# Kernel tuning notes

Hardware: AMD Instinct MI355X
Metric: run time of the kernel (lower is better)

## Reference

```python
import jax, jax.numpy as jnp
import numpy as np
import math

B, N = 1, 512
C_S, C_Z, C_H, H = 384, 128, 16, 12
P_Q, P_V, NBINS = 4, 8, 64
OUT_DIM = H * (C_H + P_V * 4 + C_Z)


def setup_inputs() -> dict:
    key = jax.random.key(0)
    ks = jax.random.split(key, 16)
    def rn(k, shape, scale=1.0):
        return jax.random.normal(k, shape, dtype=jnp.float32) * scale
    rotations, _ = jnp.linalg.qr(rn(ks[3], (B, N, 3, 3)))  # orthogonal frames
    w = 0.02
    return {
        "s": rn(ks[0], (B, N, C_S)),
        "z": rn(ks[1], (B, N, N, C_Z)),
        "translations": rn(ks[2], (B, N, 3), 10.0),  # spread over ~0-32 A bins
        "rotations": rotations,
        "Wq": rn(ks[4], (C_S, H * C_H), w), "bq": jnp.zeros((H * C_H,), jnp.float32),
        "Wk": rn(ks[5], (C_S, H * C_H), w), "bk": jnp.zeros((H * C_H,), jnp.float32),
        "Wv": rn(ks[6], (C_S, H * C_H), w), "bv": jnp.zeros((H * C_H,), jnp.float32),
        "Wqp": rn(ks[7], (C_S, H * P_Q * 3), w), "bqp": jnp.zeros((H * P_Q * 3,), jnp.float32),
        "Wkp": rn(ks[8], (C_S, H * P_Q * 3), w), "bkp": jnp.zeros((H * P_Q * 3,), jnp.float32),
        "Wvp": rn(ks[9], (C_S, H * P_V * 3), w), "bvp": jnp.zeros((H * P_V * 3,), jnp.float32),
        "Wb": rn(ks[10], (C_Z, H), w), "bb": jnp.zeros((H,), jnp.float32),
        "emb": rn(ks[11], (NBINS, H), w),
        "scale_logits": jnp.zeros((3, H), jnp.float32),
        "head_weights": jnp.ones((H,), jnp.float32),
        "Wout": rn(ks[12], (OUT_DIM, C_S), w), "bout": jnp.zeros((C_S,), jnp.float32),
    }


def reference(s, z, translations, rotations, Wq, bq, Wk, bk, Wv, bv, Wqp, bqp, Wkp, bkp, Wvp, bvp, Wb, bb, emb, scale_logits, head_weights, Wout, bout):
    b, n, _ = s.shape
    t = translations
    q = (s @ Wq + bq).reshape(b, n, H, C_H)
    k = (s @ Wk + bk).reshape(b, n, H, C_H)
    v = (s @ Wv + bv).reshape(b, n, H, C_H)
    q_pts = (s @ Wqp + bqp).reshape(b, n, H, P_Q, 3)
    k_pts = (s @ Wkp + bkp).reshape(b, n, H, P_Q, 3)
    v_pts = (s @ Wvp + bvp).reshape(b, n, H, P_V, 3)
    # local -> global frame
    q_g = jnp.einsum('bnij,bnhpj->bnhpi', rotations, q_pts) + t[:, :, None, None, :]
    k_g = jnp.einsum('bnij,bnhpj->bnhpi', rotations, k_pts) + t[:, :, None, None, :]
    v_g = jnp.einsum('bnij,bnhpj->bnhpi', rotations, v_pts) + t[:, :, None, None, :]
    scalar_logits = jnp.einsum('bnhc,bmhc->bnmh', q, k) / math.sqrt(C_H)  # [b,n,m,h]
    point_dist = jnp.sum((q_g[:, :, None] - k_g[:, None]) ** 2, axis=-1)  # [b,n,m,h,p]
    point_logits = -0.5 * jnp.sum(point_dist, axis=-1) * head_weights[None, None, None, :]
    pair_bias = z @ Wb + bb  # [b,n,m,h]
    pair_dist = jnp.linalg.norm(t[:, :, None, :] - t[:, None, :, :], axis=-1)  # [b,n,m]
    edges = jnp.linspace(0.0, 32.0, NBINS + 1)
    bins = jnp.clip(jnp.searchsorted(edges, pair_dist, side='left') - 1, 0, NBINS - 1)
    dist_bias = emb[bins]  # [b,n,m,h]
    scales = jnp.stack([
        (pair_dist <= 5.0).astype(s.dtype),
        ((pair_dist > 5.0) & (pair_dist <= 15.0)).astype(s.dtype),
        jnp.ones_like(pair_dist),
    ], axis=-1)  # [b,n,m,3]
    per_head = jax.nn.softmax(scale_logits, axis=0)  # [3,h]
    multiscale = jnp.einsum('bnms,sh->bnmh', scales, per_head)
    logits = scalar_logits + point_logits + pair_bias + dist_bias + multiscale
    attn = jax.nn.softmax(logits.astype(jnp.float32), axis=2).astype(s.dtype)  # over m
    out_scalar = jnp.einsum('bnmh,bmhc->bnhc', attn, v)
    out_pts_g = jnp.einsum('bnmh,bmhpi->bnhpi', attn, v_g)
    # global -> local frame (R^T applied)
    out_pts_l = jnp.einsum('bnji,bnhpj->bnhpi', rotations, out_pts_g - t[:, :, None, None, :])
    out_norms = jnp.linalg.norm(out_pts_l, axis=-1)  # [b,n,h,p]
    pair_feat = jnp.einsum('bnmh,bnmc->bnhc', attn, z)
    feats = jnp.concatenate([
        out_scalar,
        out_pts_l.reshape(b, n, H, P_V * 3),
        out_norms,
        pair_feat,
    ], axis=-1).reshape(b, n, -1)  # [b,n,OUT_DIM]
    return feats @ Wout + bout
```

## Files before the change

### kernel.cpp

```cpp
#include <hip/hip_runtime.h>

#define NTOK 512
#define CS 384
#define CZ 128
#define CH 16
#define HN 12
#define PQ 4
#define PV 8
#define FEAT_DIM 2112
#define HSEG 176

__global__ __launch_bounds__(256) void k_proj(
    const float* __restrict__ s,
    const float* __restrict__ Wq,  const float* __restrict__ bq,
    const float* __restrict__ Wk,  const float* __restrict__ bk,
    const float* __restrict__ Wv,  const float* __restrict__ bv,
    const float* __restrict__ Wqp, const float* __restrict__ bqp,
    const float* __restrict__ Wkp, const float* __restrict__ bkp,
    const float* __restrict__ Wvp, const float* __restrict__ bvp,
    float* __restrict__ qs, float* __restrict__ ks, float* __restrict__ vs,
    float* __restrict__ raw_g)
{
    __shared__ float s_l[16 * CS];
    const int t  = threadIdx.x;
    const int n0 = blockIdx.x * 16;

    const float4* sg  = (const float4*)(s + (size_t)n0 * CS);
    float4*       sl4 = (float4*)s_l;
#pragma unroll
    for (int j = 0; j < 6; ++j) sl4[j * 256 + t] = sg[j * 256 + t];
    __syncthreads();

    const int col = blockIdx.y * 64 + (t & 63);
    const int tq  = t >> 6;

    const float *W, *bv_;
    int lc, nc;
    if (col < 192)      { W = Wq;  bv_ = bq;  lc = col;       nc = 192; }
    else if (col < 384) { W = Wk;  bv_ = bk;  lc = col - 192; nc = 192; }
    else if (col < 576) { W = Wv;  bv_ = bv;  lc = col - 384; nc = 192; }
    else if (col < 720) { W = Wqp; bv_ = bqp; lc = col - 576; nc = 144; }
    else if (col < 864) { W = Wkp; bv_ = bkp; lc = col - 720; nc = 144; }
    else                { W = Wvp; bv_ = bvp; lc = col - 864; nc = 288; }

    const float* Wp   = W + lc;
    const float* srow = s_l + tq * 4 * CS;
    float a0, a1, a2, a3;
    a0 = a1 = a2 = a3 = bv_[lc];
#pragma unroll 8
    for (int k = 0; k < CS; ++k) {
        float w = Wp[(size_t)k * nc];
        a0 += srow[k] * w;
        a1 += srow[CS + k] * w;
        a2 += srow[2 * CS + k] * w;
        a3 += srow[3 * CS + k] * w;
    }

    const int n = n0 + tq * 4;
    if (col < 576) {
        float* dst = (col < 192 ? qs : col < 384 ? ks : vs);
        dst[(size_t)(n + 0) * 192 + lc] = a0;
        dst[(size_t)(n + 1) * 192 + lc] = a1;
        dst[(size_t)(n + 2) * 192 + lc] = a2;
        dst[(size_t)(n + 3) * 192 + lc] = a3;
    } else {
        const int pc = col - 576;
        raw_g[(size_t)(n + 0) * 576 + pc] = a0;
        raw_g[(size_t)(n + 1) * 576 + pc] = a1;
        raw_g[(size_t)(n + 2) * 576 + pc] = a2;
        raw_g[(size_t)(n + 3) * 576 + pc] = a3;
    }
}

__global__ __launch_bounds__(256) void k_frame(
    const float* __restrict__ raw_g,
    const float* __restrict__ trans,
    const float* __restrict__ rot,
    float* __restrict__ qg, float* __restrict__ kg, float* __restrict__ vg)
{
    const int e = blockIdx.x * 256 + threadIdx.x;
    const int n = e / 576, loc = e % 576;
    const int i = loc % 3, base = loc - i;
    const float* rp = raw_g + (size_t)n * 576 + base;
    float x0 = rp[0], x1 = rp[1], x2 = rp[2];
    const float* R = rot + (size_t)n * 9 + i * 3;
    float v = trans[(size_t)n * 3 + i] + R[0] * x0 + R[1] * x1 + R[2] * x2;
    if (loc < 144)      qg[(size_t)n * 144 + loc] = v;
    else if (loc < 288) kg[(size_t)n * 144 + loc - 144] = v;
    else                vg[(size_t)n * 288 + loc - 288] = v;
}

__global__ __launch_bounds__(256) void k_bias(
    const float* __restrict__ z,
    const float* __restrict__ Wb,
    const float* __restrict__ bbv,
    float* __restrict__ bias)
{
    __shared__ float a_l[64 * 132];
    __shared__ float wb_l[CZ * HN];
    __shared__ float bb_l[HN];
    const int t = threadIdx.x;
    for (int i = t; i < CZ * HN; i += 256) wb_l[i] = Wb[i];
    if (t < HN) bb_l[t] = bbv[t];

    const float4* zg = (const float4*)(z + (size_t)blockIdx.x * 64 * CZ);
#pragma unroll
    for (int j = 0; j < 8; ++j) {
        const int f4i = j * 256 + t;
        const int row = f4i >> 5, c4 = f4i & 31;
        *(float4*)&a_l[row * 132 + c4 * 4] = zg[f4i];
    }
    __syncthreads();

    const int row = t & 63;
    const int hg  = t >> 6;
    float acc0 = 0.f, acc1 = 0.f, acc2 = 0.f;
    const float4* ar = (const float4*)&a_l[row * 132];
    const float*  wr = wb_l + hg * 3;
#pragma unroll 8
    for (int k4 = 0; k4 < 32; ++k4) {
        float4 zv = ar[k4];
        float zs[4] = {zv.x, zv.y, zv.z, zv.w};
#pragma unroll
        for (int e = 0; e < 4; ++e) {
            const float* w = wr + (k4 * 4 + e) * HN;
            acc0 += zs[e] * w[0];
            acc1 += zs[e] * w[1];
            acc2 += zs[e] * w[2];
        }
    }
    const int grow = blockIdx.x * 64 + row;
    const int n = grow >> 9, m = grow & 511;
    const int h = hg * 3;
    bias[((size_t)n * HN + h + 0) * NTOK + m] = acc0 + bb_l[h + 0];
    bias[((size_t)n * HN + h + 1) * NTOK + m] = acc1 + bb_l[h + 1];
    bias[((size_t)n * HN + h + 2) * NTOK + m] = acc2 + bb_l[h + 2];
}

__global__ __launch_bounds__(256) void k_attn(
    const float* __restrict__ qs, const float* __restrict__ ks,
    const float* __restrict__ qg, const float* __restrict__ kg,
    const float* __restrict__ trans,
    const float* __restrict__ emb,
    const float* __restrict__ slog,
    const float* __restrict__ hw,
    float* __restrict__ attn)
{
    const int n = blockIdx.x, h = blockIdx.y, t = threadIdx.x;
    __shared__ float ql[CH];
    __shared__ float qgl[12];
    __shared__ float tl[3];
    __shared__ float ph[3];
    __shared__ float red[8];
    if (t < CH)       ql[t] = qs[(size_t)n * 192 + h * CH + t];
    else if (t < 28)  qgl[t - 16] = qg[(size_t)n * 144 + h * 12 + (t - 16)];
    else if (t < 31)  tl[t - 28] = trans[(size_t)n * 3 + (t - 28)];
    else if (t == 31) {
        float s0 = slog[0 * HN + h], s1 = slog[1 * HN + h], s2 = slog[2 * HN + h];
        float mx = fmaxf(s0, fmaxf(s1, s2));
        float e0 = expf(s0 - mx), e1 = expf(s1 - mx), e2 = expf(s2 - mx);
        float inv = 1.f / (e0 + e1 + e2);
        ph[0] = e0 * inv; ph[1] = e1 * inv; ph[2] = e2 * inv;
    }
    __syncthreads();

    const float hwv = hw[h];
    float* arow = attn + ((size_t)n * HN + h) * NTOK;
    float lg[2];
#pragma unroll
    for (int r = 0; r < 2; ++r) {
        const int m = t + r * 256;
        const float4* kp4 = (const float4*)(ks + (size_t)m * 192 + h * CH);
        const float4* ql4 = (const float4*)ql;
        float sc = 0.f;
#pragma unroll
        for (int c = 0; c < 4; ++c) {
            float4 kv = kp4[c], qv = ql4[c];
            sc += qv.x * kv.x + qv.y * kv.y + qv.z * kv.z + qv.w * kv.w;
        }
        sc *= 0.25f;
        const float4* kg4 = (const float4*)(kg + (size_t)m * 144 + h * 12);
        const float4* qg4 = (const float4*)qgl;
        float sd = 0.f;
#pragma unroll
        for (int u = 0; u < 3; ++u) {
            float4 kv = kg4[u], qv = qg4[u];
            float d0 = qv.x - kv.x, d1 = qv.y - kv.y, d2 = qv.z - kv.z, d3 = qv.w - kv.w;
            sd += d0 * d0 + d1 * d1 + d2 * d2 + d3 * d3;
        }
        float pl = -0.5f * sd * hwv;
        float dx = tl[0] - trans[(size_t)m * 3 + 0];
        float dy = tl[1] - trans[(size_t)m * 3 + 1];
        float dz = tl[2] - trans[(size_t)m * 3 + 2];
        float dist = sqrtf(dx * dx + dy * dy + dz * dz);
        int bin = (int)ceilf(dist * 2.f) - 1;
        bin = min(63, max(0, bin));
        float db = emb[bin * HN + h];
        float ms = ph[2] + (dist <= 5.f ? ph[0] : 0.f) + ((dist > 5.f && dist <= 15.f) ? ph[1] : 0.f);
        lg[r] = sc + pl + arow[m] + db + ms;
    }

    float mx = fmaxf(lg[0], lg[1]);
    for (int off = 32; off; off >>= 1) mx = fmaxf(mx, __shfl_down(mx, off));
    if ((t & 63) == 0) red[t >> 6] = mx;
    __syncthreads();
    if (t == 0) red[4] = fmaxf(fmaxf(red[0], red[1]), fmaxf(red[2], red[3]));
    __syncthreads();
    mx = red[4];
    float e0 = expf(lg[0] - mx), e1 = expf(lg[1] - mx);
    float sm = e0 + e1;
    for (int off = 32; off; off >>= 1) sm += __shfl_down(sm, off);
    if ((t & 63) == 0) red[t >> 6] = sm;
    __syncthreads();
    if (t == 0) red[5] = red[0] + red[1] + red[2] + red[3];
    __syncthreads();
    const float inv = 1.f / red[5];
    arow[t] = e0 * inv;
    arow[t + 256] = e1 * inv;
}

__global__ __launch_bounds__(256) void k_out_partial(
    const float* __restrict__ attn,
    const float* __restrict__ vs, const float* __restrict__ vg,
    float* __restrict__ sums_g)
{
    __shared__ float a_l[HN * 128];
    const int n = blockIdx.x, mc = blockIdx.y, t = threadIdx.x;
    for (int i = t; i < HN * 128; i += 256) {
        const int h = i >> 7, mm = i & 127;
        a_l[i] = attn[((size_t)n * HN + h) * NTOK + mc * 128 + mm];
    }
    __syncthreads();

    const int mbase = mc * 128;
    const int o0 = t;
    const int o1raw = t + 256;
    const bool act1 = o1raw < 480;
    const int o1 = act1 ? o1raw : 0;
    const int h0 = o0 / 40, j0 = o0 % 40;
    const int h1 = o1 / 40, j1 = o1 % 40;
    const float* b0; int st0;
    if (j0 < 16) { b0 = vs + h0 * 16 + j0;        st0 = 192; }
    else         { b0 = vg + h0 * 24 + (j0 - 16); st0 = 288; }
    const float* b1; int st1;
    if (j1 < 16) { b1 = vs + h1 * 16 + j1;        st1 = 192; }
    else         { b1 = vg + h1 * 24 + (j1 - 16); st1 = 288; }
    b0 += (size_t)mbase * st0;
    b1 += (size_t)mbase * st1;
    const float* a0 = a_l + h0 * 128;
    const float* a1 = a_l + h1 * 128;
    float acc0 = 0.f, acc1 = 0.f;
#pragma unroll 8
    for (int m = 0; m < 128; ++m) {
        acc0 += a0[m] * b0[(size_t)m * st0];
        acc1 += a1[m] * b1[(size_t)m * st1];
    }
    atomicAdd(&sums_g[(size_t)n * 480 + o0], acc0);
    if (act1) atomicAdd(&sums_g[(size_t)n * 480 + o1raw], acc1);
}

__global__ __launch_bounds__(256) void k_out_epi(
    const float* __restrict__ sums_g,
    const float* __restrict__ trans,
    const float* __restrict__ rot,
    float* __restrict__ feats)
{
    __shared__ float sums[480];
    __shared__ float Rl[9];
    __shared__ float tl[3];
    const int n = blockIdx.x, t = threadIdx.x;
    for (int i = t; i < 480; i += 256) sums[i] = sums_g[(size_t)n * 480 + i];
    if (t < 9)       Rl[t] = rot[(size_t)n * 9 + t];
    else if (t < 12) tl[t - 9] = trans[(size_t)n * 3 + (t - 9)];
    __syncthreads();

    for (int f = t; f < 576; f += 256) {
        const int h = f / 48, j = f % 48;
        float* fp = feats + (size_t)n * FEAT_DIM + h * HSEG;
        const float* sh = sums + h * 40;
        if (j < 16) {
            fp[j] = sh[j];
        } else if (j < 40) {
            int jj = j - 16, p = jj / 3, i = jj % 3;
            float val = 0.f;
#pragma unroll
            for (int q = 0; q < 3; ++q) val += Rl[q * 3 + i] * (sh[16 + p * 3 + q] - tl[q]);
            fp[16 + jj] = val;
        } else {
            int p = j - 40;
            float s2 = 0.f;
#pragma unroll
            for (int i = 0; i < 3; ++i) {
                float val = 0.f;
#pragma unroll
                for (int q = 0; q < 3; ++q) val += Rl[q * 3 + i] * (sh[16 + p * 3 + q] - tl[q]);
                s2 += val * val;
            }
            fp[40 + p] = sqrtf(s2);
        }
    }
}

__global__ __launch_bounds__(256) void k_pairfeat(
    const float* __restrict__ attn,
    const float* __restrict__ z,
    float* __restrict__ feats)
{
    __shared__ float a_l[HN * NTOK];
    const int n = blockIdx.x, t = threadIdx.x;
    for (int i = t; i < HN * NTOK; i += 256) a_l[i] = attn[(size_t)n * HN * NTOK + i];
    __syncthreads();

    const int c2 = (t & 63) * 2;
    const int hb = (t >> 6) * 3;
    float acc[3][2] = {{0.f, 0.f}, {0.f, 0.f}, {0.f, 0.f}};
    const float* zp = z + (size_t)n * NTOK * CZ + c2;
    const float* ap = a_l + hb * NTOK;
#pragma unroll 4
    for (int m = 0; m < NTOK; ++m) {
        float2 zv = *(const float2*)(zp + (size_t)m * CZ);
#pragma unroll
        for (int u = 0; u < 3; ++u) {
            float a = ap[u * NTOK + m];
            acc[u][0] += a * zv.x;
            acc[u][1] += a * zv.y;
        }
    }
#pragma unroll
    for (int u = 0; u < 3; ++u) {
        float2 r = make_float2(acc[u][0], acc[u][1]);
        *(float2*)&feats[(size_t)n * FEAT_DIM + (hb + u) * HSEG + 48 + c2] = r;
    }
}

#define KT 16
__global__ __launch_bounds__(256) void k_outproj(
    const float* __restrict__ feats,
    const float* __restrict__ Wout,
    const float* __restrict__ bout,
    float* __restrict__ out)
{
    __shared__ float As[KT][64];
    __shared__ float Bs[KT][64];
    const int t  = threadIdx.x;
    const int n0 = blockIdx.x * 64;
    const int j0 = blockIdx.y * 64;
    const int k0 = blockIdx.z * HSEG;

    const int arow = t >> 2, akq = (t & 3) * 4;
    const int bkk  = t >> 4, bjq = (t & 15) * 4;
    const int tr   = t >> 4, tc  = t & 15;

    float acc[4][4] = {{0.f}};
    for (int s = 0; s < 11; ++s) {
        const int ks = k0 + s * KT;
        float4 a4 = *(const float4*)&feats[(size_t)(n0 + arow) * FEAT_DIM + ks + akq];
        float4 b4 = *(const float4*)&Wout[(size_t)(ks + bkk) * 384 + j0 + bjq];
        __syncthreads();
        As[akq + 0][arow] = a4.x;
        As[akq + 1][arow] = a4.y;
        As[akq + 2][arow] = a4.z;
        As[akq + 3][arow] = a4.w;
        *(float4*)&Bs[bkk][bjq] = b4;
        __syncthreads();
// ... 24 lines not shown
            atomicAdd(&out[(size_t)row * 384 + col], v);
        }
    }
}

extern "C" void kernel_launch(void* const* d_in, const int* in_sizes, int n_in,
                              void* d_out, int out_size, void* d_ws, size_t ws_size,
                              hipStream_t stream) {
    const float* s     = (const float*)d_in[0];
    const float* z     = (const float*)d_in[1];
    const float* trans = (const float*)d_in[2];
    const float* rot   = (const float*)d_in[3];
    const float* Wq    = (const float*)d_in[4];
    const float* bq    = (const float*)d_in[5];
    const float* Wk    = (const float*)d_in[6];
    const float* bk    = (const float*)d_in[7];
    const float* Wv    = (const float*)d_in[8];
    const float* bv    = (const float*)d_in[9];
    const float* Wqp   = (const float*)d_in[10];
    const float* bqp   = (const float*)d_in[11];
    const float* Wkp   = (const float*)d_in[12];
    const float* bkp   = (const float*)d_in[13];
    const float* Wvp   = (const float*)d_in[14];
    const float* bvp   = (const float*)d_in[15];
    const float* Wb    = (const float*)d_in[16];
    const float* bb    = (const float*)d_in[17];
    const float* emb   = (const float*)d_in[18];
    const float* slog  = (const float*)d_in[19];
    const float* hw    = (const float*)d_in[20];
    const float* Wout  = (const float*)d_in[21];
    const float* bout  = (const float*)d_in[22];

    float* W = (float*)d_ws;
    float* qs    = W;
    float* ks    = qs + 98304;
    float* vs    = ks + 98304;
    float* qg    = vs + 98304;
    float* kg    = qg + 73728;
    float* vg    = kg + 73728;
    float* bias  = vg + 147456;
    float* feats = bias + 3145728;
    float* raw_g = feats + 1081344;
    float* sums_g = raw_g;

    k_proj<<<dim3(32, 18), 256, 0, stream>>>(s, Wq, bq, Wk, bk, Wv, bv,
                                             Wqp, bqp, Wkp, bkp, Wvp, bvp,
                                             qs, ks, vs, raw_g);
    k_frame<<<1152, 256, 0, stream>>>(raw_g, trans, rot, qg, kg, vg);
    hipMemsetAsync(sums_g, 0, (size_t)NTOK * 480 * sizeof(float), stream);
    k_bias<<<4096, 256, 0, stream>>>(z, Wb, bb, bias);
    k_attn<<<dim3(512, 12), 256, 0, stream>>>(qs, ks, qg, kg, trans, emb, slog, hw, bias);
    k_out_partial<<<dim3(512, 4), 256, 0, stream>>>(bias, vs, vg, sums_g);
    k_out_epi<<<512, 256, 0, stream>>>(sums_g, trans, rot, feats);
    k_pairfeat<<<512, 256, 0, stream>>>(bias, z, feats);
    hipMemsetAsync(d_out, 0, (size_t)NTOK * 384 * sizeof(float), stream);
    k_outproj<<<dim3(8, 6, 12), 256, 0, stream>>>(feats, Wout, bout, (float*)d_out);
}
```

Measured before the change: 460.8 us.

## Transpose key tensors for coalesced attention and tile the value aggregation

The projection and frame kernels now write keys, key points and translations in transposed (feature-major) layouts, so adjacent threads in the attention kernel read consecutive keys with coalesced loads. The distance-embedding column is staged in shared memory. The atomic partial-sum plus epilogue pair for the attention-weighted values is replaced by one register-tiled kernel per 64-token tile and head, which also does the frame transform and removes a memset. The new value kernel launches only 96 blocks, so the GPU may be underfilled.

```diff
diff --git a/kernel.cpp b/kernel.cpp
--- a/kernel.cpp
+++ b/kernel.cpp
@@ -18,7 +18,7 @@
     const float* __restrict__ Wqp, const float* __restrict__ bqp,
     const float* __restrict__ Wkp, const float* __restrict__ bkp,
     const float* __restrict__ Wvp, const float* __restrict__ bvp,
-    float* __restrict__ qs, float* __restrict__ ks, float* __restrict__ vs,
+    float* __restrict__ qs, float* __restrict__ ksT, float* __restrict__ vs,
     float* __restrict__ raw_g)
 {
     __shared__ float s_l[16 * CS];
@@ -57,12 +57,19 @@
     }
 
     const int n = n0 + tq * 4;
-    if (col < 576) {
-        float* dst = (col < 192 ? qs : col < 384 ? ks : vs);
-        dst[(size_t)(n + 0) * 192 + lc] = a0;
-        dst[(size_t)(n + 1) * 192 + lc] = a1;
-        dst[(size_t)(n + 2) * 192 + lc] = a2;
-        dst[(size_t)(n + 3) * 192 + lc] = a3;
+    if (col < 192) {
+        qs[(size_t)(n + 0) * 192 + lc] = a0;
+        qs[(size_t)(n + 1) * 192 + lc] = a1;
+        qs[(size_t)(n + 2) * 192 + lc] = a2;
+        qs[(size_t)(n + 3) * 192 + lc] = a3;
+    } else if (col < 384) {
+        float* p = ksT + (size_t)lc * NTOK + n;
+        p[0] = a0; p[1] = a1; p[2] = a2; p[3] = a3;
+    } else if (col < 576) {
+        vs[(size_t)(n + 0) * 192 + lc] = a0;
+        vs[(size_t)(n + 1) * 192 + lc] = a1;
+        vs[(size_t)(n + 2) * 192 + lc] = a2;
+        vs[(size_t)(n + 3) * 192 + lc] = a3;
     } else {
         const int pc = col - 576;
         raw_g[(size_t)(n + 0) * 576 + pc] = a0;
@@ -76,18 +83,27 @@
     const float* __restrict__ raw_g,
     const float* __restrict__ trans,
     const float* __restrict__ rot,
-    float* __restrict__ qg, float* __restrict__ kg, float* __restrict__ vg)
+    float* __restrict__ qg, float* __restrict__ kgT, float* __restrict__ vg,
+    float* __restrict__ transT)
 {
     const int e = blockIdx.x * 256 + threadIdx.x;
-    const int n = e / 576, loc = e % 576;
-    const int i = loc % 3, base = loc - i;
-    const float* rp = raw_g + (size_t)n * 576 + base;
-    float x0 = rp[0], x1 = rp[1], x2 = rp[2];
-    const float* R = rot + (size_t)n * 9 + i * 3;
-    float v = trans[(size_t)n * 3 + i] + R[0] * x0 + R[1] * x1 + R[2] * x2;
-    if (loc < 144)      qg[(size_t)n * 144 + loc] = v;
-    else if (loc < 288) kg[(size_t)n * 144 + loc - 144] = v;
-    else                vg[(size_t)n * 288 + loc - 288] = v;
+    if (e < 512 * 576) {
+        const int n = e / 576, loc = e % 576;
+        const int i = loc % 3, base = loc - i;
+        const float* rp = raw_g + (size_t)n * 576 + base;
+        float x0 = rp[0], x1 = rp[1], x2 = rp[2];
+        const float* R = rot + (size_t)n * 9 + i * 3;
+        float v = trans[(size_t)n * 3 + i] + R[0] * x0 + R[1] * x1 + R[2] * x2;
+        if (loc < 144)      qg[(size_t)n * 144 + loc] = v;
+        else if (loc < 288) kgT[(size_t)(loc - 144) * NTOK + n] = v;
+        else                vg[(size_t)n * 288 + loc - 288] = v;
+    } else {
+        const int idx = e - 512 * 576;
+        if (idx < 3 * NTOK) {
+            const int m = idx / 3, i = idx % 3;
+            transT[(size_t)i * NTOK + m] = trans[(size_t)m * 3 + i];
+        }
+    }
 }
 
 __global__ __launch_bounds__(256) void k_bias(
@@ -138,9 +154,9 @@
 }
 
 __global__ __launch_bounds__(256) void k_attn(
-    const float* __restrict__ qs, const float* __restrict__ ks,
-    const float* __restrict__ qg, const float* __restrict__ kg,
-    const float* __restrict__ trans,
+    const float* __restrict__ qs, const float* __restrict__ ksT,
+    const float* __restrict__ qg, const float* __restrict__ kgT,
+    const float* __restrict__ trans, const float* __restrict__ transT,
     const float* __restrict__ emb,
     const float* __restrict__ slog,
     const float* __restrict__ hw,
@@ -152,6 +168,7 @@
     __shared__ float tl[3];
     __shared__ float ph[3];
     __shared__ float red[8];
+    __shared__ float emb_l[64];
     if (t < CH)       ql[t] = qs[(size_t)n * 192 + h * CH + t];
     else if (t < 28)  qgl[t - 16] = qg[(size_t)n * 144 + h * 12 + (t - 16)];
     else if (t < 31)  tl[t - 28] = trans[(size_t)n * 3 + (t - 28)];
@@ -161,41 +178,38 @@
         float e0 = expf(s0 - mx), e1 = expf(s1 - mx), e2 = expf(s2 - mx);
         float inv = 1.f / (e0 + e1 + e2);
         ph[0] = e0 * inv; ph[1] = e1 * inv; ph[2] = e2 * inv;
+    } else if (t >= 64 && t < 128) {
+        emb_l[t - 64] = emb[(size_t)(t - 64) * HN + h];
     }
     __syncthreads();
 
     const float hwv = hw[h];
     float* arow = attn + ((size_t)n * HN + h) * NTOK;
+    const float* ksh = ksT + (size_t)h * CH * NTOK;
+    const float* kgh = kgT + (size_t)h * 12 * NTOK;
     float lg[2];
 #pragma unroll
     for (int r = 0; r < 2; ++r) {
         const int m = t + r * 256;
-        const float4* kp4 = (const float4*)(ks + (size_t)m * 192 + h * CH);
-        const float4* ql4 = (const float4*)ql;
         float sc = 0.f;
 #pragma unroll
-        for (int c = 0; c < 4; ++c) {
-            float4 kv = kp4[c], qv = ql4[c];
-            sc += qv.x * kv.x + qv.y * kv.y + qv.z * kv.z + qv.w * kv.w;
-        }
+        for (int c = 0; c < CH; ++c)
+            sc += ql[c] * ksh[(size_t)c * NTOK + m];
         sc *= 0.25f;
-        const float4* kg4 = (const float4*)(kg + (size_t)m * 144 + h * 12);
-        const float4* qg4 = (const float4*)qgl;
         float sd = 0.f;
 #pragma unroll
-        for (int u = 0; u < 3; ++u) {
-            float4 kv = kg4[u], qv = qg4[u];
-            float d0 = qv.x - kv.x, d1 = qv.y - kv.y, d2 = qv.z - kv.z, d3 = qv.w - kv.w;
-            sd += d0 * d0 + d1 * d1 + d2 * d2 + d3 * d3;
+        for (int i = 0; i < 12; ++i) {
+            float d = qgl[i] - kgh[(size_t)i * NTOK + m];
+            sd += d * d;
         }
         float pl = -0.5f * sd * hwv;
-        float dx = tl[0] - trans[(size_t)m * 3 + 0];
-        float dy = tl[1] - trans[(size_t)m * 3 + 1];
-        float dz = tl[2] - trans[(size_t)m * 3 + 2];
+        float dx = tl[0] - transT[m];
+        float dy = tl[1] - transT[NTOK + m];
+        float dz = tl[2] - transT[2 * NTOK + m];
         float dist = sqrtf(dx * dx + dy * dy + dz * dz);
         int bin = (int)ceilf(dist * 2.f) - 1;
         bin = min(63, max(0, bin));
-        float db = emb[bin * HN + h];
+        float db = emb_l[bin];
         float ms = ph[2] + (dist <= 5.f ? ph[0] : 0.f) + ((dist > 5.f && dist <= 15.f) ? ph[1] : 0.f);
         lg[r] = sc + pl + arow[m] + db + ms;
     }
@@ -219,81 +233,118 @@
     arow[t + 256] = e1 * inv;
 }
 
-__global__ __launch_bounds__(256) void k_out_partial(
+__global__ __launch_bounds__(256) void k_outmm(
     const float* __restrict__ attn,
     const float* __restrict__ vs, const float* __restrict__ vg,
-    float* __restrict__ sums_g)
-{
-    __shared__ float a_l[HN * 128];
-    const int n = blockIdx.x, mc = blockIdx.y, t = threadIdx.x;
-    for (int i = t; i < HN * 128; i += 256) {
-        const int h = i >> 7, mm = i & 127;
-        a_l[i] = attn[((size_t)n * HN + h) * NTOK + mc * 128 + mm];
-    }
-    __syncthreads();
-
-    const int mbase = mc * 128;
-    const int o0 = t;
-    const int o1raw = t + 256;
-    const bool act1 = o1raw < 480;
-    const int o1 = act1 ? o1raw : 0;
-    const int h0 = o0 / 40, j0 = o0 % 40;
-    const int h1 = o1 / 40, j1 = o1 % 40;
-    const float* b0; int st0;
-    if (j0 < 16) { b0 = vs + h0 * 16 + j0;        st0 = 192; }
-    else         { b0 = vg + h0 * 24 + (j0 - 16); st0 = 288; }
-    const float* b1; int st1;
-    if (j1 < 16) { b1 = vs + h1 * 16 + j1;        st1 = 192; }
-    else         { b1 = vg + h1 * 24 + (j1 - 16); st1 = 288; }
-    b0 += (size_t)mbase * st0;
-    b1 += (size_t)mbase * st1;
-    const float* a0 = a_l + h0 * 128;
-    const float* a1 = a_l + h1 * 128;
-    float acc0 = 0.f, acc1 = 0.f;
-#pragma unroll 8
-    for (int m = 0; m < 128; ++m) {
-        acc0 += a0[m] * b0[(size_t)m * st0];
-        acc1 += a1[m] * b1[(size_t)m * st1];
-    }
-    atomicAdd(&sums_g[(size_t)n * 480 + o0], acc0);
-    if (act1) atomicAdd(&sums_g[(size_t)n * 480 + o1raw], acc1);
-}
-
-__global__ __launch_bounds__(256) void k_out_epi(
-    const float* __restrict__ sums_g,
     const float* __restrict__ trans,
     const float* __restrict__ rot,
     float* __restrict__ feats)
 {
-    __shared__ float sums[480];
-    __shared__ float Rl[9];
-    __shared__ float tl[3];
-    const int n = blockIdx.x, t = threadIdx.x;
-    for (int i = t; i < 480; i += 256) sums[i] = sums_g[(size_t)n * 480 + i];
-    if (t < 9)       Rl[t] = rot[(size_t)n * 9 + t];
-    else if (t < 12) tl[t - 9] = trans[(size_t)n * 3 + (t - 9)];
-    __syncthreads();
-
-    for (int f = t; f < 576; f += 256) {
-        const int h = f / 48, j = f % 48;
-        float* fp = feats + (size_t)n * FEAT_DIM + h * HSEG;
-        const float* sh = sums + h * 40;
+    __shared__ float As_t[64][65];
+    __shared__ float Vs[64][40];
+    __shared__ float out_l[64 * 40];
+    __shared__ float Rl[64][9];
+    __shared__ float tl[64][3];
+    const int t   = threadIdx.x;
+    const int gn0 = blockIdx.x * 64;
+    const int h   = blockIdx.y;
+
+    const int slab  = t >> 6;
+    const int w     = t & 63;
+    const int n0l   = (w >> 2) * 4;
+    const int j0    = (w & 3) * 10;
+
+    float acc[4][10];
+#pragma unroll
+    for (int i = 0; i < 4; ++i)
+#pragma unroll
+        for (int k = 0; k < 10; ++k) acc[i][k] = 0.f;
+
+    for (int step = 0; step < 8; ++step) {
+        const int mb = step * 64;
+        __syncthreads();
+#pragma unroll
+        for (int jj = 0; jj < 4; ++jj) {
+            const int f = t + jj * 256;
+            const int n_loc = f >> 4, c4 = f & 15;
+            float4 a = *(const float4*)&attn[(((size_t)(gn0 + n_loc)) * HN + h) * NTOK + mb + c4 * 4];
+            As_t[c4 * 4 + 0][n_loc] = a.x;
+            As_t[c4 * 4 + 1][n_loc] = a.y;
+            As_t[c4 * 4 + 2][n_loc] = a.z;
+            As_t[c4 * 4 + 3][n_loc] = a.w;
+        }
+#pragma unroll
+        for (int jj = 0; jj < 10; ++jj) {
+            const int f = t + jj * 256;
+            const int m_loc = f / 40, jv = f % 40;
+            float v;
+            if (jv < 16) v = vs[(size_t)(mb + m_loc) * 192 + h * 16 + jv];
+            else         v = vg[(size_t)(mb + m_loc) * 288 + h * 24 + (jv - 16)];
+            Vs[m_loc][jv] = v;
+        }
+        __syncthreads();
+#pragma unroll
+        for (int mi = 0; mi < 16; ++mi) {
+            const int m = slab * 16 + mi;
+            float4 a  = *(const float4*)&As_t[m][n0l];
+            float2 v0 = *(const float2*)&Vs[m][j0 + 0];
+            float2 v1 = *(const float2*)&Vs[m][j0 + 2];
+            float2 v2 = *(const float2*)&Vs[m][j0 + 4];
+            float2 v3 = *(const float2*)&Vs[m][j0 + 6];
+            float2 v4 = *(const float2*)&Vs[m][j0 + 8];
+            const float av[4]  = {a.x, a.y, a.z, a.w};
+            const float vv[10] = {v0.x, v0.y, v1.x, v1.y, v2.x,
+                                  v2.y, v3.x, v3.y, v4.x, v4.y};
+#pragma unroll
+            for (int i = 0; i < 4; ++i)
+#pragma unroll
+                for (int k = 0; k < 10; ++k)
+                    acc[i][k] += av[i] * vv[k];
+        }
+    }
+
+    for (int s = 0; s < 4; ++s) {
+        __syncthreads();
+        if (slab == s) {
+#pragma unroll
+            for (int i = 0; i < 4; ++i)
+#pragma unroll
+                for (int k = 0; k < 10; ++k) {
+                    float* p = &out_l[(n0l + i) * 40 + j0 + k];
+                    if (s == 0) *p = acc[i][k];
+                    else        *p += acc[i][k];
+                }
+        }
+    }
+    for (int i = t; i < 64 * 12; i += 256) {
+        const int n_loc = i / 12, r = i % 12;
+        if (r < 9) Rl[n_loc][r] = rot[(size_t)(gn0 + n_loc) * 9 + r];
+        else       tl[n_loc][r - 9] = trans[(size_t)(gn0 + n_loc) * 3 + (r - 9)];
+    }
+    __syncthreads();
+
+    for (int f = t; f < 64 * 48; f += 256) {
+        const int n_loc = f / 48, j = f % 48;
+        const float* sh = &out_l[n_loc * 40];
+        float* fp = feats + (size_t)(gn0 + n_loc) * FEAT_DIM + h * HSEG;
+        const float* R = Rl[n_loc];
+        const float* tv = tl[n_loc];
         if (j < 16) {
             fp[j] = sh[j];
         } else if (j < 40) {
-            int jj = j - 16, p = jj / 3, i = jj % 3;
+            const int jj = j - 16, p = jj / 3, i = jj % 3;
             float val = 0.f;
 #pragma unroll
-            for (int q = 0; q < 3; ++q) val += Rl[q * 3 + i] * (sh[16 + p * 3 + q] - tl[q]);
+            for (int q = 0; q < 3; ++q) val += R[q * 3 + i] * (sh[16 + p * 3 + q] - tv[q]);
             fp[16 + jj] = val;
         } else {
-            int p = j - 40;
+            const int p = j - 40;
             float s2 = 0.f;
 #pragma unroll
             for (int i = 0; i < 3; ++i) {
                 float val = 0.f;
 #pragma unroll
-                for (int q = 0; q < 3; ++q) val += Rl[q * 3 + i] * (sh[16 + p * 3 + q] - tl[q]);
+                for (int q = 0; q < 3; ++q) val += R[q * 3 + i] * (sh[16 + p * 3 + q] - tv[q]);
                 s2 += val * val;
             }
             fp[40 + p] = sqrtf(s2);
@@ -316,7 +367,7 @@
     float acc[3][2] = {{0.f, 0.f}, {0.f, 0.f}, {0.f, 0.f}};
     const float* zp = z + (size_t)n * NTOK * CZ + c2;
     const float* ap = a_l + hb * NTOK;
-#pragma unroll 4
+#pragma unroll 8
     for (int m = 0; m < NTOK; ++m) {
         float2 zv = *(const float2*)(zp + (size_t)m * CZ);
 #pragma unroll
@@ -420,26 +471,25 @@
     const float* bout  = (const float*)d_in[22];
 
     float* W = (float*)d_ws;
-    float* qs    = W;
-    float* ks    = qs + 98304;
-    float* vs    = ks + 98304;
-    float* qg    = vs + 98304;
-    float* kg    = qg + 73728;
-    float* vg    = kg + 73728;
-    float* bias  = vg + 147456;
-    float* feats = bias + 3145728;
-    float* raw_g = feats + 1081344;
-    float* sums_g = raw_g;
+    float* qs     = W;
+    float* ksT    = qs + 98304;
+    float* vs     = ksT + 98304;
+    float* qg     = vs + 98304;
+    float* kgT    = qg + 73728;
+    float* vg     = kgT + 73728;
+    float* transT = vg + 147456;
+    float* bias   = transT + 1536;
+    float* feats  = bias + 3145728;
+    float* raw_g  = feats + 1081344;
 
     k_proj<<<dim3(32, 18), 256, 0, stream>>>(s, Wq, bq, Wk, bk, Wv, bv,
                                              Wqp, bqp, Wkp, bkp, Wvp, bvp,
-                                             qs, ks, vs, raw_g);
-    k_frame<<<1152, 256, 0, stream>>>(raw_g, trans, rot, qg, kg, vg);
-    hipMemsetAsync(sums_g, 0, (size_t)NTOK * 480 * sizeof(float), stream);
+                                             qs, ksT, vs, raw_g);
+    k_frame<<<1158, 256, 0, stream>>>(raw_g, trans, rot, qg, kgT, vg, transT);
     k_bias<<<4096, 256, 0, stream>>>(z, Wb, bb, bias);
-    k_attn<<<dim3(512, 12), 256, 0, stream>>>(qs, ks, qg, kg, trans, emb, slog, hw, bias);
-    k_out_partial<<<dim3(512, 4), 256, 0, stream>>>(bias, vs, vg, sums_g);
-    k_out_epi<<<512, 256, 0, stream>>>(sums_g, trans, rot, feats);
+    k_attn<<<dim3(512, 12), 256, 0, stream>>>(qs, ksT, qg, kgT, trans, transT,
+                                              emb, slog, hw, bias);
+    k_outmm<<<dim3(8, 12), 256, 0, stream>>>(bias, vs, vg, trans, rot, feats);
     k_pairfeat<<<512, 256, 0, stream>>>(bias, z, feats);
     hipMemsetAsync(d_out, 0, (size_t)NTOK * 384 * sizeof(float), stream);
     k_outproj<<<dim3(8, 6, 12), 256, 0, stream>>>(feats, Wout, bout, (float*)d_out);
```

Measured after the change: 415.9 us. -9.7%, faster.

## Fuse pair bias, attention, softmax, and aggregation into one per-token mega kernel

Applied to the files above, without the earlier changes.

Projection and frame transform are merged into one kernel that writes K, K-points, and V in transposed layouts. Pair bias, logits, softmax, value/point aggregation, and pair-feature reduction are fused into a single per-query-token block that keeps the 12x512 attention row in shared memory. This removes the global bias/attention round-trips, the atomics and their memset, and several launches. The cost is a large shared-memory footprint per block (lower occupancy), only 512 blocks, and z being read twice within the block.

```diff
diff --git a/kernel.cpp b/kernel.cpp
--- a/kernel.cpp
+++ b/kernel.cpp
@@ -5,289 +5,306 @@
 #define CZ 128
 #define CH 16
 #define HN 12
-#define PQ 4
-#define PV 8
 #define FEAT_DIM 2112
 #define HSEG 176
 
-__global__ __launch_bounds__(256) void k_proj(
+__global__ __launch_bounds__(256) void k_projframe(
     const float* __restrict__ s,
+    const float* __restrict__ trans,
+    const float* __restrict__ rot,
     const float* __restrict__ Wq,  const float* __restrict__ bq,
     const float* __restrict__ Wk,  const float* __restrict__ bk,
     const float* __restrict__ Wv,  const float* __restrict__ bv,
     const float* __restrict__ Wqp, const float* __restrict__ bqp,
     const float* __restrict__ Wkp, const float* __restrict__ bkp,
     const float* __restrict__ Wvp, const float* __restrict__ bvp,
-    float* __restrict__ qs, float* __restrict__ ks, float* __restrict__ vs,
-    float* __restrict__ raw_g)
+    float* __restrict__ qs, float* __restrict__ ksT,
+    float* __restrict__ qg, float* __restrict__ kgT,
+    float* __restrict__ VT, float* __restrict__ transT)
 {
-    __shared__ float s_l[16 * CS];
+    __shared__ float s_l[8 * CS];
+    __shared__ float raw_l[8 * 576];
+    __shared__ float Rt_l[8][12];
     const int t  = threadIdx.x;
-    const int n0 = blockIdx.x * 16;
+    const int n0 = blockIdx.x * 8;
+    const int half = blockIdx.y;
 
     const float4* sg  = (const float4*)(s + (size_t)n0 * CS);
     float4*       sl4 = (float4*)s_l;
 #pragma unroll
-    for (int j = 0; j < 6; ++j) sl4[j * 256 + t] = sg[j * 256 + t];
-    __syncthreads();
-
-    const int col = blockIdx.y * 64 + (t & 63);
-    const int tq  = t >> 6;
-
-    const float *W, *bv_;
-    int lc, nc;
-    if (col < 192)      { W = Wq;  bv_ = bq;  lc = col;       nc = 192; }
-    else if (col < 384) { W = Wk;  bv_ = bk;  lc = col - 192; nc = 192; }
-    else if (col < 576) { W = Wv;  bv_ = bv;  lc = col - 384; nc = 192; }
-    else if (col < 720) { W = Wqp; bv_ = bqp; lc = col - 576; nc = 144; }
-    else if (col < 864) { W = Wkp; bv_ = bkp; lc = col - 720; nc = 144; }
-    else                { W = Wvp; bv_ = bvp; lc = col - 864; nc = 288; }
-
-    const float* Wp   = W + lc;
-    const float* srow = s_l + tq * 4 * CS;
-    float a0, a1, a2, a3;
-    a0 = a1 = a2 = a3 = bv_[lc];
+    for (int j = 0; j < 3; ++j) sl4[j * 256 + t] = sg[j * 256 + t];
+    if (half == 1 && t < 96) {
+        const int tok = t / 12, r = t % 12;
+        if (r < 9) Rt_l[tok][r] = rot[(size_t)(n0 + tok) * 9 + r];
+        else       Rt_l[tok][r] = trans[(size_t)(n0 + tok) * 3 + (r - 9)];
+    }
+    __syncthreads();
+
+    for (int c = t; c < 576; c += 256) {
+        const float* W; const float* bp; int lc, nc;
+        if (half == 0) {
+            if (c < 192)      { W = Wq; bp = bq; lc = c;       }
+            else if (c < 384) { W = Wk; bp = bk; lc = c - 192; }
+            else              { W = Wv; bp = bv; lc = c - 384; }
+            nc = 192;
+        } else {
+            if (c < 144)      { W = Wqp; bp = bqp; lc = c;       nc = 144; }
+            else if (c < 288) { W = Wkp; bp = bkp; lc = c - 144; nc = 144; }
+            else              { W = Wvp; bp = bvp; lc = c - 288; nc = 288; }
+        }
+        float a[8];
+        const float bias = bp[lc];
+#pragma unroll
+        for (int i = 0; i < 8; ++i) a[i] = bias;
+        const float* Wp = W + lc;
 #pragma unroll 8
-    for (int k = 0; k < CS; ++k) {
-        float w = Wp[(size_t)k * nc];
-        a0 += srow[k] * w;
-        a1 += srow[CS + k] * w;
-        a2 += srow[2 * CS + k] * w;
-        a3 += srow[3 * CS + k] * w;
-    }
-
-    const int n = n0 + tq * 4;
-    if (col < 576) {
-        float* dst = (col < 192 ? qs : col < 384 ? ks : vs);
-        dst[(size_t)(n + 0) * 192 + lc] = a0;
-        dst[(size_t)(n + 1) * 192 + lc] = a1;
-        dst[(size_t)(n + 2) * 192 + lc] = a2;
-        dst[(size_t)(n + 3) * 192 + lc] = a3;
-    } else {
-        const int pc = col - 576;
-        raw_g[(size_t)(n + 0) * 576 + pc] = a0;
-        raw_g[(size_t)(n + 1) * 576 + pc] = a1;
-        raw_g[(size_t)(n + 2) * 576 + pc] = a2;
-        raw_g[(size_t)(n + 3) * 576 + pc] = a3;
+        for (int k = 0; k < CS; ++k) {
+            float w = Wp[(size_t)k * nc];
+#pragma unroll
+            for (int i = 0; i < 8; ++i) a[i] += s_l[i * CS + k] * w;
+        }
+        if (half == 0) {
+            if (c < 192) {
+#pragma unroll
+                for (int i = 0; i < 8; ++i) qs[(size_t)(n0 + i) * 192 + lc] = a[i];
+            } else if (c < 384) {
+                float* p = ksT + (size_t)lc * NTOK + n0;
+#pragma unroll
+                for (int i = 0; i < 8; ++i) p[i] = a[i];
+            } else {
+                const int vrow = (lc >> 4) * 40 + (lc & 15);
+                float* p = VT + (size_t)vrow * NTOK + n0;
+#pragma unroll
+                for (int i = 0; i < 8; ++i) p[i] = a[i];
+            }
+        } else {
+#pragma unroll
+            for (int i = 0; i < 8; ++i) raw_l[i * 576 + c] = a[i];
+        }
+    }
+
+    if (half == 1) {
+        __syncthreads();
+        for (int f = t; f < 8 * 576; f += 256) {
+            const int tok = f / 576, loc = f % 576;
+            const int i = loc % 3, base = loc - i;
+            const float* x = &raw_l[tok * 576 + base];
+            const float* R = &Rt_l[tok][i * 3];
+            float v = Rt_l[tok][9 + i] + R[0] * x[0] + R[1] * x[1] + R[2] * x[2];
+            const int n = n0 + tok;
+            if (loc < 144)      qg[(size_t)n * 144 + loc] = v;
+            else if (loc < 288) kgT[(size_t)(loc - 144) * NTOK + n] = v;
+            else {
+                const int pc = loc - 288;
+                const int vrow = (pc / 24) * 40 + 16 + (pc % 24);
+                VT[(size_t)vrow * NTOK + n] = v;
+            }
+        }
+        if (t < 24) {
+            const int tok = t % 8, i = t / 8;
+            transT[(size_t)i * NTOK + n0 + tok] = trans[(size_t)(n0 + tok) * 3 + i];
+        }
     }
 }
 
-__global__ __launch_bounds__(256) void k_frame(
-    const float* __restrict__ raw_g,
-    const float* __restrict__ trans,
+__global__ __launch_bounds__(256) void k_mega(
+    const float* __restrict__ z,
+    const float* __restrict__ qs, const float* __restrict__ ksT,
+    const float* __restrict__ qg, const float* __restrict__ kgT,
+    const float* __restrict__ VT,
+    const float* __restrict__ trans, const float* __restrict__ transT,
     const float* __restrict__ rot,
-    float* __restrict__ qg, float* __restrict__ kg, float* __restrict__ vg)
+    const float* __restrict__ Wb, const float* __restrict__ bbv,
+    const float* __restrict__ emb, const float* __restrict__ slog,
+    const float* __restrict__ hw,
+    float* __restrict__ feats)
 {
-    const int e = blockIdx.x * 256 + threadIdx.x;
-    const int n = e / 576, loc = e % 576;
-    const int i = loc % 3, base = loc - i;
-    const float* rp = raw_g + (size_t)n * 576 + base;
-    float x0 = rp[0], x1 = rp[1], x2 = rp[2];
-    const float* R = rot + (size_t)n * 9 + i * 3;
-    float v = trans[(size_t)n * 3 + i] + R[0] * x0 + R[1] * x1 + R[2] * x2;
-    if (loc < 144)      qg[(size_t)n * 144 + loc] = v;
-    else if (loc < 288) kg[(size_t)n * 144 + loc - 144] = v;
-    else                vg[(size_t)n * 288 + loc - 288] = v;
-}
-
-__global__ __launch_bounds__(256) void k_bias(
-    const float* __restrict__ z,
-    const float* __restrict__ Wb,
-    const float* __restrict__ bbv,
-    float* __restrict__ bias)
-{
-    __shared__ float a_l[64 * 132];
-    __shared__ float wb_l[CZ * HN];
-    __shared__ float bb_l[HN];
-    const int t = threadIdx.x;
-    for (int i = t; i < CZ * HN; i += 256) wb_l[i] = Wb[i];
-    if (t < HN) bb_l[t] = bbv[t];
-
-    const float4* zg = (const float4*)(z + (size_t)blockIdx.x * 64 * CZ);
-#pragma unroll
-    for (int j = 0; j < 8; ++j) {
-        const int f4i = j * 256 + t;
-        const int row = f4i >> 5, c4 = f4i & 31;
-        *(float4*)&a_l[row * 132 + c4 * 4] = zg[f4i];
-    }
-    __syncthreads();
-
-    const int row = t & 63;
-    const int hg  = t >> 6;
-    float acc0 = 0.f, acc1 = 0.f, acc2 = 0.f;
-    const float4* ar = (const float4*)&a_l[row * 132];
-    const float*  wr = wb_l + hg * 3;
-#pragma unroll 8
-    for (int k4 = 0; k4 < 32; ++k4) {
-        float4 zv = ar[k4];
-        float zs[4] = {zv.x, zv.y, zv.z, zv.w};
-#pragma unroll
-        for (int e = 0; e < 4; ++e) {
-            const float* w = wr + (k4 * 4 + e) * HN;
-            acc0 += zs[e] * w[0];
-            acc1 += zs[e] * w[1];
-            acc2 += zs[e] * w[2];
-        }
-    }
-    const int grow = blockIdx.x * 64 + row;
-    const int n = grow >> 9, m = grow & 511;
-    const int h = hg * 3;
-    bias[((size_t)n * HN + h + 0) * NTOK + m] = acc0 + bb_l[h + 0];
-    bias[((size_t)n * HN + h + 1) * NTOK + m] = acc1 + bb_l[h + 1];
-    bias[((size_t)n * HN + h + 2) * NTOK + m] = acc2 + bb_l[h + 2];
-}
-
-__global__ __launch_bounds__(256) void k_attn(
-    const float* __restrict__ qs, const float* __restrict__ ks,
-    const float* __restrict__ qg, const float* __restrict__ kg,
-    const float* __restrict__ trans,
-    const float* __restrict__ emb,
-    const float* __restrict__ slog,
-    const float* __restrict__ hw,
-    float* __restrict__ attn)
-{
-    const int n = blockIdx.x, h = blockIdx.y, t = threadIdx.x;
-    __shared__ float ql[CH];
-    __shared__ float qgl[12];
-    __shared__ float tl[3];
-    __shared__ float ph[3];
-    __shared__ float red[8];
-    if (t < CH)       ql[t] = qs[(size_t)n * 192 + h * CH + t];
-    else if (t < 28)  qgl[t - 16] = qg[(size_t)n * 144 + h * 12 + (t - 16)];
-    else if (t < 31)  tl[t - 28] = trans[(size_t)n * 3 + (t - 28)];
-    else if (t == 31) {
-        float s0 = slog[0 * HN + h], s1 = slog[1 * HN + h], s2 = slog[2 * HN + h];
+    __shared__ float att[HN * NTOK];
+    __shared__ float scratch[64 * 133];
+    __shared__ float emb_l[64 * HN];
+    __shared__ float q_l[192], qg_l[144];
+    __shared__ float ph_l[36], hw_l[HN], bb_l[HN];
+    __shared__ float Rl[9], tl[3];
+    __shared__ float outl[480];
+    const int n = blockIdx.x, t = threadIdx.x;
+
+    for (int i = t; i < 64 * HN; i += 256) emb_l[i] = emb[i];
+    if (t < 192) q_l[t] = qs[(size_t)n * 192 + t];
+    if (t < 144) qg_l[t] = qg[(size_t)n * 144 + t];
+    if (t < HN) {
+        bb_l[t] = bbv[t]; hw_l[t] = hw[t];
+        float s0 = slog[t], s1 = slog[HN + t], s2 = slog[2 * HN + t];
         float mx = fmaxf(s0, fmaxf(s1, s2));
         float e0 = expf(s0 - mx), e1 = expf(s1 - mx), e2 = expf(s2 - mx);
-        float inv = 1.f / (e0 + e1 + e2);
-        ph[0] = e0 * inv; ph[1] = e1 * inv; ph[2] = e2 * inv;
-    }
-    __syncthreads();
-
-    const float hwv = hw[h];
-    float* arow = attn + ((size_t)n * HN + h) * NTOK;
-    float lg[2];
+        float iv = 1.f / (e0 + e1 + e2);
+        ph_l[t] = e0 * iv; ph_l[HN + t] = e1 * iv; ph_l[2 * HN + t] = e2 * iv;
+    }
+    if (t < 9) Rl[t] = rot[(size_t)n * 9 + t];
+    if (t >= 16 && t < 19) tl[t - 16] = trans[(size_t)n * 3 + (t - 16)];
+    __syncthreads();
+
+    {
+        const int m1  = t & 63;
+        const int hg1 = __builtin_amdgcn_readfirstlane(t >> 6);
+        const float* wbp = Wb + hg1 * 3;
+        for (int ch = 0; ch < 8; ++ch) {
+            const int mb = ch * 64;
+            if (ch) __syncthreads();
+#pragma unroll
+            for (int j = 0; j < 8; ++j) {
+                const int f = t + j * 256;
+                const int row = f >> 5, c4 = f & 31;
+                float4 v = *(const float4*)&z[((size_t)n * NTOK + mb + row) * CZ + c4 * 4];
+                float* d = &scratch[row * 133 + c4 * 4];
+                d[0] = v.x; d[1] = v.y; d[2] = v.z; d[3] = v.w;
+            }
+            __syncthreads();
+            float a0 = 0.f, a1 = 0.f, a2 = 0.f;
+            const float* zr = &scratch[m1 * 133];
+#pragma unroll 4
+            for (int c4 = 0; c4 < 32; ++c4) {
+                float4 zq = *(const float4*)&zr[c4 * 4];
+                const float zs[4] = {zq.x, zq.y, zq.z, zq.w};
+#pragma unroll
+                for (int e = 0; e < 4; ++e) {
+                    const float* w = wbp + (c4 * 4 + e) * HN;
+                    a0 += zs[e] * w[0];
+                    a1 += zs[e] * w[1];
+                    a2 += zs[e] * w[2];
+                }
+            }
+            att[(hg1 * 3 + 0) * NTOK + mb + m1] = a0 + bb_l[hg1 * 3 + 0];
+            att[(hg1 * 3 + 1) * NTOK + mb + m1] = a1 + bb_l[hg1 * 3 + 1];
+            att[(hg1 * 3 + 2) * NTOK + mb + m1] = a2 + bb_l[hg1 * 3 + 2];
+        }
+    }
+    __syncthreads();
+
 #pragma unroll
     for (int r = 0; r < 2; ++r) {
         const int m = t + r * 256;
-        const float4* kp4 = (const float4*)(ks + (size_t)m * 192 + h * CH);
-        const float4* ql4 = (const float4*)ql;
-        float sc = 0.f;
-#pragma unroll
-        for (int c = 0; c < 4; ++c) {
-            float4 kv = kp4[c], qv = ql4[c];
-            sc += qv.x * kv.x + qv.y * kv.y + qv.z * kv.z + qv.w * kv.w;
-        }
-        sc *= 0.25f;
-        const float4* kg4 = (const float4*)(kg + (size_t)m * 144 + h * 12);
-        const float4* qg4 = (const float4*)qgl;
-        float sd = 0.f;
-#pragma unroll
-        for (int u = 0; u < 3; ++u) {
-            float4 kv = kg4[u], qv = qg4[u];
-            float d0 = qv.x - kv.x, d1 = qv.y - kv.y, d2 = qv.z - kv.z, d3 = qv.w - kv.w;
-            sd += d0 * d0 + d1 * d1 + d2 * d2 + d3 * d3;
-        }
-        float pl = -0.5f * sd * hwv;
-        float dx = tl[0] - trans[(size_t)m * 3 + 0];
-        float dy = tl[1] - trans[(size_t)m * 3 + 1];
-        float dz = tl[2] - trans[(size_t)m * 3 + 2];
-        float dist = sqrtf(dx * dx + dy * dy + dz * dz);
+        const float dx = tl[0] - transT[m];
+        const float dy = tl[1] - transT[NTOK + m];
+        const float dz = tl[2] - transT[2 * NTOK + m];
+        const float dist = sqrtf(dx * dx + dy * dy + dz * dz);
         int bin = (int)ceilf(dist * 2.f) - 1;
         bin = min(63, max(0, bin));
-        float db = emb[bin * HN + h];
-        float ms = ph[2] + (dist <= 5.f ? ph[0] : 0.f) + ((dist > 5.f && dist <= 15.f) ? ph[1] : 0.f);
-        lg[r] = sc + pl + arow[m] + db + ms;
-    }
-
-    float mx = fmaxf(lg[0], lg[1]);
-    for (int off = 32; off; off >>= 1) mx = fmaxf(mx, __shfl_down(mx, off));
-    if ((t & 63) == 0) red[t >> 6] = mx;
-    __syncthreads();
-    if (t == 0) red[4] = fmaxf(fmaxf(red[0], red[1]), fmaxf(red[2], red[3]));
-    __syncthreads();
-    mx = red[4];
-    float e0 = expf(lg[0] - mx), e1 = expf(lg[1] - mx);
-    float sm = e0 + e1;
-    for (int off = 32; off; off >>= 1) sm += __shfl_down(sm, off);
-    if ((t & 63) == 0) red[t >> 6] = sm;
-    __syncthreads();
-    if (t == 0) red[5] = red[0] + red[1] + red[2] + red[3];
-    __syncthreads();
-    const float inv = 1.f / red[5];
-    arow[t] = e0 * inv;
-    arow[t + 256] = e1 * inv;
-}
-
-__global__ __launch_bounds__(256) void k_out_partial(
-    const float* __restrict__ attn,
-    const float* __restrict__ vs, const float* __restrict__ vg,
-    float* __restrict__ sums_g)
-{
-    __shared__ float a_l[HN * 128];
-    const int n = blockIdx.x, mc = blockIdx.y, t = threadIdx.x;
-    for (int i = t; i < HN * 128; i += 256) {
-        const int h = i >> 7, mm = i & 127;
-        a_l[i] = attn[((size_t)n * HN + h) * NTOK + mc * 128 + mm];
-    }
-    __syncthreads();
-
-    const int mbase = mc * 128;
-    const int o0 = t;
-    const int o1raw = t + 256;
-    const bool act1 = o1raw < 480;
-    const int o1 = act1 ? o1raw : 0;
-    const int h0 = o0 / 40, j0 = o0 % 40;
-    const int h1 = o1 / 40, j1 = o1 % 40;
-    const float* b0; int st0;
-    if (j0 < 16) { b0 = vs + h0 * 16 + j0;        st0 = 192; }
-    else         { b0 = vg + h0 * 24 + (j0 - 16); st0 = 288; }
-    const float* b1; int st1;
-    if (j1 < 16) { b1 = vs + h1 * 16 + j1;        st1 = 192; }
-    else         { b1 = vg + h1 * 24 + (j1 - 16); st1 = 288; }
-    b0 += (size_t)mbase * st0;
-    b1 += (size_t)mbase * st1;
-    const float* a0 = a_l + h0 * 128;
-    const float* a1 = a_l + h1 * 128;
-    float acc0 = 0.f, acc1 = 0.f;
-#pragma unroll 8
-    for (int m = 0; m < 128; ++m) {
-        acc0 += a0[m] * b0[(size_t)m * st0];
-        acc1 += a1[m] * b1[(size_t)m * st1];
-    }
-    atomicAdd(&sums_g[(size_t)n * 480 + o0], acc0);
-    if (act1) atomicAdd(&sums_g[(size_t)n * 480 + o1raw], acc1);
-}
-
-__global__ __launch_bounds__(256) void k_out_epi(
-    const float* __restrict__ sums_g,
-    const float* __restrict__ trans,
-    const float* __restrict__ rot,
-    float* __restrict__ feats)
-{
-    __shared__ float sums[480];
-    __shared__ float Rl[9];
-    __shared__ float tl[3];
-    const int n = blockIdx.x, t = threadIdx.x;
-    for (int i = t; i < 480; i += 256) sums[i] = sums_g[(size_t)n * 480 + i];
-    if (t < 9)       Rl[t] = rot[(size_t)n * 9 + t];
-    else if (t < 12) tl[t - 9] = trans[(size_t)n * 3 + (t - 9)];
-    __syncthreads();
-
+        const bool in0 = (dist <= 5.f), in1 = (dist > 5.f && dist <= 15.f);
+        for (int h = 0; h < HN; ++h) {
+            float sc = 0.f;
+#pragma unroll
+            for (int c = 0; c < CH; ++c)
+                sc += q_l[h * CH + c] * ksT[(size_t)(h * CH + c) * NTOK + m];
+            float sd = 0.f;
+#pragma unroll
+            for (int i = 0; i < 12; ++i) {
+                float d = qg_l[h * 12 + i] - kgT[(size_t)(h * 12 + i) * NTOK + m];
+                sd += d * d;
+            }
+            float ms = ph_l[2 * HN + h] + (in0 ? ph_l[h] : 0.f) + (in1 ? ph_l[HN + h] : 0.f);
+            att[h * NTOK + m] = sc * 0.25f - 0.5f * sd * hw_l[h]
+                              + att[h * NTOK + m] + emb_l[bin * HN + h] + ms;
+        }
+    }
+    __syncthreads();
+
+    {
+        const int wv = t >> 6, lane = t & 63;
+        for (int u = 0; u < 3; ++u) {
+            const int h = wv * 3 + u;
+            float v[8]; float mx = -1e30f;
+#pragma unroll
+            for (int k = 0; k < 8; ++k) { v[k] = att[h * NTOK + lane + 64 * k]; mx = fmaxf(mx, v[k]); }
+#pragma unroll
+            for (int off = 32; off; off >>= 1) mx = fmaxf(mx, __shfl_xor(mx, off));
+            float sm = 0.f;
+#pragma unroll
+            for (int k = 0; k < 8; ++k) { v[k] = expf(v[k] - mx); sm += v[k]; }
+#pragma unroll
+            for (int off = 32; off; off >>= 1) sm += __shfl_xor(sm, off);
+            const float inv = 1.f / sm;
+#pragma unroll
+            for (int k = 0; k < 8; ++k) att[h * NTOK + lane + 64 * k] = v[k] * inv;
+        }
+    }
+    __syncthreads();
+
+    {
+        const int wv = __builtin_amdgcn_readfirstlane(t >> 6);
+        const int lane = t & 63;
+        for (int u = 0; u < 3; ++u) {
+            const int h = wv * 3 + u;
+            float av[8];
+#pragma unroll
+            for (int k = 0; k < 8; ++k) av[k] = att[h * NTOK + lane + 64 * k];
+            for (int j = 0; j < 40; ++j) {
+                const float* vrow = VT + (size_t)(h * 40 + j) * NTOK + lane;
+                float a = 0.f;
+#pragma unroll
+                for (int k = 0; k < 8; ++k) a += av[k] * vrow[64 * k];
+#pragma unroll
+                for (int off = 32; off; off >>= 1) a += __shfl_down(a, off);
+                if (lane == 0) outl[h * 40 + j] = a;
+            }
+        }
+    }
+
+    {
+        const int slab = t >> 6;
+        const int lane = t & 63;
+        const int hgp  = lane >> 5;
+        const int cq   = lane & 31;
+        float acc[6][4];
+#pragma unroll
+        for (int u = 0; u < 6; ++u)
+#pragma unroll
+            for (int v = 0; v < 4; ++v) acc[u][v] = 0.f;
+        const int mbase = slab * 128;
+        for (int m4 = 0; m4 < 128; m4 += 4) {
+            float4 a4[6];
+#pragma unroll
+            for (int u = 0; u < 6; ++u)
+                a4[u] = *(const float4*)&att[(hgp * 6 + u) * NTOK + mbase + m4];
+#pragma unroll
+            for (int mi = 0; mi < 4; ++mi) {
+                const int m = mbase + m4 + mi;
+                float4 zq = *(const float4*)&z[((size_t)n * NTOK + m) * CZ + cq * 4];
+                const float zs[4] = {zq.x, zq.y, zq.z, zq.w};
+#pragma unroll
+                for (int u = 0; u < 6; ++u) {
+                    const float am = ((const float*)&a4[u])[mi];
+#pragma unroll
+                    for (int v = 0; v < 4; ++v) acc[u][v] += am * zs[v];
+                }
+            }
+        }
+#pragma unroll
+        for (int u = 0; u < 6; ++u) {
+            float* p = &scratch[slab * 1536 + (hgp * 6 + u) * CZ + cq * 4];
+            p[0] = acc[u][0]; p[1] = acc[u][1]; p[2] = acc[u][2]; p[3] = acc[u][3];
+        }
+    }
+    __syncthreads();
+
+    for (int f = t; f < HN * CZ; f += 256) {
+        const int h = f >> 7, c = f & 127;
+        float sum = scratch[f] + scratch[1536 + f] + scratch[3072 + f] + scratch[4608 + f];
+        feats[(size_t)n * FEAT_DIM + h * HSEG + 48 + c] = sum;
+    }
     for (int f = t; f < 576; f += 256) {
         const int h = f / 48, j = f % 48;
+        const float* sh = &outl[h * 40];
         float* fp = feats + (size_t)n * FEAT_DIM + h * HSEG;
-        const float* sh = sums + h * 40;
         if (j < 16) {
             fp[j] = sh[j];
         } else if (j < 40) {
-            int jj = j - 16, p = jj / 3, i = jj % 3;
+            const int jj = j - 16, p = jj / 3, i = jj % 3;
             float val = 0.f;
 #pragma unroll
             for (int q = 0; q < 3; ++q) val += Rl[q * 3 + i] * (sh[16 + p * 3 + q] - tl[q]);
             fp[16 + jj] = val;
         } else {
-            int p = j - 40;
+            const int p = j - 40;
             float s2 = 0.f;
 #pragma unroll
             for (int i = 0; i < 3; ++i) {
@@ -298,38 +315,6 @@
             }
             fp[40 + p] = sqrtf(s2);
         }
-    }
-}
-
-__global__ __launch_bounds__(256) void k_pairfeat(
-    const float* __restrict__ attn,
-    const float* __restrict__ z,
-    float* __restrict__ feats)
-{
-    __shared__ float a_l[HN * NTOK];
-    const int n = blockIdx.x, t = threadIdx.x;
-    for (int i = t; i < HN * NTOK; i += 256) a_l[i] = attn[(size_t)n * HN * NTOK + i];
-    __syncthreads();
-
-    const int c2 = (t & 63) * 2;
-    const int hb = (t >> 6) * 3;
-    float acc[3][2] = {{0.f, 0.f}, {0.f, 0.f}, {0.f, 0.f}};
-    const float* zp = z + (size_t)n * NTOK * CZ + c2;
-    const float* ap = a_l + hb * NTOK;
-#pragma unroll 4
-    for (int m = 0; m < NTOK; ++m) {
-        float2 zv = *(const float2*)(zp + (size_t)m * CZ);
-#pragma unroll
-        for (int u = 0; u < 3; ++u) {
-            float a = ap[u * NTOK + m];
-            acc[u][0] += a * zv.x;
-            acc[u][1] += a * zv.y;
-        }
-    }
-#pragma unroll
-    for (int u = 0; u < 3; ++u) {
-        float2 r = make_float2(acc[u][0], acc[u][1]);
-        *(float2*)&feats[(size_t)n * FEAT_DIM + (hb + u) * HSEG + 48 + c2] = r;
     }
 }
 
@@ -420,27 +405,21 @@
     const float* bout  = (const float*)d_in[22];
 
     float* W = (float*)d_ws;
-    float* qs    = W;
-    float* ks    = qs + 98304;
-    float* vs    = ks + 98304;
-    float* qg    = vs + 98304;
-    float* kg    = qg + 73728;
-    float* vg    = kg + 73728;
-    float* bias  = vg + 147456;
-    float* feats = bias + 3145728;
-    float* raw_g = feats + 1081344;
-    float* sums_g = raw_g;
-
-    k_proj<<<dim3(32, 18), 256, 0, stream>>>(s, Wq, bq, Wk, bk, Wv, bv,
-                                             Wqp, bqp, Wkp, bkp, Wvp, bvp,
-                                             qs, ks, vs, raw_g);
-    k_frame<<<1152, 256, 0, stream>>>(raw_g, trans, rot, qg, kg, vg);
-    hipMemsetAsync(sums_g, 0, (size_t)NTOK * 480 * sizeof(float), stream);
-    k_bias<<<4096, 256, 0, stream>>>(z, Wb, bb, bias);
-    k_attn<<<dim3(512, 12), 256, 0, stream>>>(qs, ks, qg, kg, trans, emb, slog, hw, bias);
-    k_out_partial<<<dim3(512, 4), 256, 0, stream>>>(bias, vs, vg, sums_g);
-    k_out_epi<<<512, 256, 0, stream>>>(sums_g, trans, rot, feats);
-    k_pairfeat<<<512, 256, 0, stream>>>(bias, z, feats);
+    float* qs     = W;
+    float* ksT    = qs + 98304;
+    float* qg     = ksT + 98304;
+    float* kgT    = qg + 73728;
+    float* VT     = kgT + 73728;
+    float* transT = VT + 245760;
+    float* feats  = transT + 1536;
+
+    k_projframe<<<dim3(64, 2), 256, 0, stream>>>(
+        s, trans, rot, Wq, bq, Wk, bk, Wv, bv,
+        Wqp, bqp, Wkp, bkp, Wvp, bvp,
+        qs, ksT, qg, kgT, VT, transT);
+    k_mega<<<512, 256, 0, stream>>>(
+        z, qs, ksT, qg, kgT, VT, trans, transT, rot,
+        Wb, bb, emb, slog, hw, feats);
     hipMemsetAsync(d_out, 0, (size_t)NTOK * 384 * sizeof(float), stream);
     k_outproj<<<dim3(8, 6, 12), 256, 0, stream>>>(feats, Wout, bout, (float*)d_out);
 }
```

After: 847.7 us. +84.0%, slower.
